# Performance work log

Measured on AMD Instinct MI355X. Metric: run time of the kernel, lower is better.

Reference implementation:

```python
import jax, jax.numpy as jnp
import numpy as np

N_ATOMS = 16384
APC = 64            # atoms per conformer
N_CONF = 256        # 64 mols * 4 confs
N_MOL = 64
DEG = 32
E = N_ATOMS * DEG
H = 128             # hidden_channels = num_filters = out_channels
G = 50              # num_gaussians
L = 6               # num_interactions
CUTOFF = 10.0
LOG2 = float(np.log(2.0))


def ssp(x):
    # ShiftedSoftplus: softplus(x) - log(2)
    return jax.nn.softplus(x) - LOG2


def setup_inputs() -> dict:
    key = jax.random.key(0)
    ks = jax.random.split(key, 24)
    rng = np.random.default_rng(0)

    z = jnp.asarray(rng.integers(1, 100, size=(N_ATOMS,)), dtype=jnp.int64 if jax.config.jax_enable_x64 else jnp.int32)
    # positions uniform in a 5A box -> all intra-conformer distances < cutoff
    pos = jax.random.uniform(ks[0], (N_ATOMS, 3), dtype=jnp.float32) * 5.0

    # within-conformer random edges, no self loops (radius_graph surrogate)
    i = np.repeat(np.arange(N_ATOMS), DEG)
    off = rng.integers(1, APC, size=E)
    j = (i // APC) * APC + (i % APC + off) % APC
    edge_index = jnp.asarray(np.stack([j, i]), dtype=jnp.int32)  # [2,E] (source, target)

    atom_to_conf = jnp.asarray(np.arange(N_ATOMS) // APC, dtype=jnp.int32)
    conf_to_mol = jnp.asarray(np.arange(N_CONF) // (N_CONF // N_MOL), dtype=jnp.int32)

    s = 0.05
    p = {
        'emb':     jax.random.normal(ks[1], (120, H), jnp.float32) * s,
        # per-interaction stacked params [L, ...]
        'mlp_w1':  jax.random.normal(ks[2], (L, G, H), jnp.float32) * s,
        'mlp_b1':  jnp.zeros((L, H), jnp.float32),
        'mlp_w2':  jax.random.normal(ks[3], (L, H, H), jnp.float32) * s,
        'mlp_b2':  jnp.zeros((L, H), jnp.float32),
        'cf_w1':   jax.random.normal(ks[4], (L, H, H), jnp.float32) * s,
        'cf_w2':   jax.random.normal(ks[5], (L, H, H), jnp.float32) * s,
        'cf_b2':   jnp.zeros((L, H), jnp.float32),
        'int_w':   jax.random.normal(ks[6], (L, H, H), jnp.float32) * s,
        'int_b':   jnp.zeros((L, H), jnp.float32),
        # readout head
        'out_w1':  jax.random.normal(ks[7], (H, H), jnp.float32) * s,
        'out_b1':  jnp.zeros((H,), jnp.float32),
        'out_w2':  jax.random.normal(ks[8], (H, H), jnp.float32) * s,
        'out_b2':  jnp.zeros((H,), jnp.float32),
        'head_w1': jax.random.normal(ks[9], (H, H // 2), jnp.float32) * s,
        'head_b1': jnp.zeros((H // 2,), jnp.float32),
        'head_w2': jax.random.normal(ks[10], (H // 2, 1), jnp.float32) * s,
        'head_b2': jnp.zeros((1,), jnp.float32),
    }
    return dict(z=z, pos=pos, edge_index=edge_index, atom_to_conf=atom_to_conf,
                conf_to_mol=conf_to_mol, **p)


def reference(z, pos, edge_index, atom_to_conf, conf_to_mol, emb,
              mlp_w1, mlp_b1, mlp_w2, mlp_b2, cf_w1, cf_w2, cf_b2,
              int_w, int_b, out_w1, out_b1, out_w2, out_b2,
              head_w1, head_b1, head_w2, head_b2):
    row, col = edge_index[0], edge_index[1]  # message from row, aggregated at col

    h = emb[z]                                             # [N,H]
    edge_weight = jnp.linalg.norm(pos[row] - pos[col], axis=-1)  # [E]

    # GaussianSmearing
    offset = jnp.linspace(0.0, CUTOFF, G)
    coeff = -0.5 / (offset[1] - offset[0]) ** 2
    edge_attr = jnp.exp(coeff * (edge_weight[:, None] - offset[None, :]) ** 2)  # [E,G]

    C = 0.5 * (jnp.cos(edge_weight * jnp.pi / CUTOFF) + 1.0)  # cosine cutoff [E]

    for l in range(L):
        # filter network on edge features, modulated by cutoff envelope
        Wf = ssp(edge_attr @ mlp_w1[l] + mlp_b1[l]) @ mlp_w2[l] + mlp_b2[l]
        Wf = Wf * C[:, None]                               # [E,H]
        xf = h @ cf_w1[l]                                  # lin1 (no bias) [N,H]
        msg = xf[row] * Wf                                 # gather * filter [E,H]
        agg = jax.ops.segment_sum(msg, col, num_segments=N_ATOMS)  # scatter-add [N,H]
        xc = agg @ cf_w2[l] + cf_b2[l]                     # lin2
        h = h + (ssp(xc) @ int_w[l] + int_b[l])            # act, lin, residual

    h = ssp(h @ out_w1 + out_b1)
    h = h @ out_w2 + out_b2                                # [N,H]

    conf_emb = jax.ops.segment_sum(h, atom_to_conf, num_segments=N_CONF)   # [C,H]
    mol_emb = jax.ops.segment_sum(conf_emb, conf_to_mol, num_segments=N_MOL)  # [M,H]

    out = (ssp(mol_emb @ head_w1 + head_b1) @ head_w2 + head_b2)[:, 0]  # [M]
    return out
```

## Files before the change

kernel.cpp:

```cpp
#include <hip/hip_runtime.h>
#include <math.h>

#define N_ATOMS 16384
#define APC 64
#define N_CONF 256
#define N_MOL 64
#define DEG 32
#define NEDGE (N_ATOMS * DEG)
#define H 128
#define G 50
#define NL 6
#define TP0 512
#define TPB 4096
#define CUTOFF 10.0f

typedef __attribute__((ext_vector_type(8))) short short8_t;
typedef __attribute__((ext_vector_type(4))) float f32x4;
typedef __attribute__((ext_vector_type(2))) float f32x2;

__device__ __forceinline__ float ssp_f(float x) {
  float e = __expf(-fabsf(x));
  return fmaxf(x, 0.f) + __logf(1.f + e) - 0.69314718055994531f;
}
__device__ __forceinline__ unsigned short bf16_rne(float x) {
  unsigned u = __float_as_uint(x);
  unsigned r = u + 0x7FFF + ((u >> 16) & 1);
  return (unsigned short)(r >> 16);
}
__device__ __forceinline__ float bf16_to_f(unsigned short s) {
  return __uint_as_float(((unsigned)s) << 16);
}
__device__ __forceinline__ float bflo(unsigned u) { return __uint_as_float(u << 16); }
__device__ __forceinline__ float bfhi(unsigned u) { return __uint_as_float(u & 0xFFFF0000u); }

__device__ __forceinline__ unsigned cvt_pk_bf16(float a, float b) {
  unsigned r;
  asm("v_cvt_pk_bf16_f32 %0, %1, %2" : "=v"(r) : "v"(a), "v"(b));
  return r;
}
__device__ __forceinline__ void pack4(const f32x4 v, uint2* hh, uint2* ll) {
  unsigned h01 = cvt_pk_bf16(v[0], v[1]);
  unsigned h23 = cvt_pk_bf16(v[2], v[3]);
  unsigned l01 = cvt_pk_bf16(v[0] - bflo(h01), v[1] - bfhi(h01));
  unsigned l23 = cvt_pk_bf16(v[2] - bflo(h23), v[3] - bfhi(h23));
  *hh = make_uint2(h01, h23);
  *ll = make_uint2(l01, l23);
}

__global__ __launch_bounds__(256) void k_setup(
    const float* __restrict__ pos, const int* __restrict__ esrc,
    const int* __restrict__ etgt, int* __restrict__ pk,
    const float* __restrict__ cf_w1, const float* __restrict__ cf_w2,
    const float* __restrict__ int_w, const float* __restrict__ out_w1,
    const float* __restrict__ out_w2, short* __restrict__ PW,
    const float* __restrict__ w1, const float* __restrict__ b1,
    const float* __restrict__ w2, const float* __restrict__ b2,
    float* __restrict__ T, int* __restrict__ cnt) {
  __shared__ float g2[2][64];
  __shared__ float S2[2][128];
  const int b = blockIdx.x;
  const int tid = threadIdx.x;
  if (b == 0 && tid == 0) *cnt = 0;
  if (b < 2048) {
    int e = b * 256 + tid;
    int r = esrc[e], c = etgt[e];
    float dx = pos[r * 3 + 0] - pos[c * 3 + 0];
    float dy = pos[r * 3 + 1] - pos[c * 3 + 1];
    float dz = pos[r * 3 + 2] - pos[c * 3 + 2];
    float d = sqrtf(dx * dx + dy * dy + dz * dz);
    int i = (int)(d * ((float)(TPB - 1) / CUTOFF) + 0.5f);
    if (i > TPB - 1) i = TPB - 1;
    if (i < 0) i = 0;
    pk[e] = (i << 8) | ((r & (APC - 1)) << 20);
  } else if (b < 2208) {
    int e = (b - 2048) * 256 + tid;
    int g = e >> 11, t = e & 2047;
    int kb = t >> 9, rem = t & 511, nt = rem >> 6, lane = rem & 63;
    int quad = lane >> 4, ln = lane & 15;
    int kbase = kb * 32 + quad * 8;
    int n = nt * 16 + ln;
    const float* src;
    if (g < 12) {
      int l = g >> 1;
      src = (g & 1) ? (int_w + l * 16384) : (cf_w2 + l * 16384);
    } else if (g < 18) {
      src = cf_w1 + (g - 12) * 16384;
    } else {
      src = (g == 18) ? out_w1 : out_w2;
    }
    short hv[8], lv[8];
    #pragma unroll
    for (int j = 0; j < 8; j++) {
      float x = src[(kbase + j) * H + n];
      unsigned short hb = bf16_rne(x);
      hv[j] = (short)hb;
      lv[j] = (short)bf16_rne(x - bf16_to_f(hb));
    }
    size_t base = (size_t)g * 32768 + (size_t)t * 8;
    *(short8_t*)&PW[base] = *(short8_t*)hv;
    *(short8_t*)&PW[base + 16384] = *(short8_t*)lv;
  } else {
    int bb = b - 2208;
    const int l = bb >> 8;
    const int grp = tid >> 7;
    const int c = tid & 127;
    const int p = (bb & 255) * 2 + grp;
    const float d = (float)p * (CUTOFF / (float)(TP0 - 1));
    const float gspace = CUTOFF / (float)(G - 1);
    const float coeff = -0.5f / (gspace * gspace);
    if (c < G) {
      float x = d - (float)c * gspace;
      g2[grp][c] = __expf(coeff * x * x);
    }
    __syncthreads();
    const float* W1 = w1 + l * G * H;
    float s = b1[l * H + c];
    #pragma unroll 5
    for (int i = 0; i < G; i++) s += g2[grp][i] * W1[i * H + c];
    S2[grp][c] = ssp_f(s);
    __syncthreads();
    const float* W2 = w2 + l * H * H;
    float o = b2[l * H + c];
    #pragma unroll 8
    for (int j = 0; j < H; j++) o += S2[grp][j] * W2[j * H + c];
    float Cc = 0.5f * (__cosf(d * (3.14159265358979f / CUTOFF)) + 1.f);
    T[((size_t)l * TP0 + p) * H + c] = o * Cc;
  }
}

__global__ __launch_bounds__(256) void k_up(const float* __restrict__ T,
                                            unsigned short* __restrict__ Tb) {
  int t = blockIdx.x * 256 + threadIdx.x;
  int l = t >> 17;
  int rem = t & 131071;
  int p4 = rem >> 5, cg = rem & 31;
  int c = cg * 4;
  float u = (float)p4 * ((float)(TP0 - 1) / (float)(TPB - 1));
  int i = (int)u;
  if (i > TP0 - 2) i = TP0 - 2;
  float f = u - (float)i;
  const float* a = T + ((size_t)l * TP0 + i) * H + c;
  float4 v0 = *(const float4*)a;
  float4 v1 = *(const float4*)(a + H);
  ushort4 o;
  o.x = bf16_rne(v0.x + f * (v1.x - v0.x));
  o.y = bf16_rne(v0.y + f * (v1.y - v0.y));
  o.z = bf16_rne(v0.z + f * (v1.z - v0.z));
  o.w = bf16_rne(v0.w + f * (v1.w - v0.w));
  int dst = (cg < 16) ? cg * 8 : (cg - 16) * 8 + 4;
  *(ushort4*)&Tb[((size_t)l * TPB + p4) * H + dst] = o;
}

#define MFMA(a, b, c) __builtin_amdgcn_mfma_f32_16x16x32_bf16((a), (b), (c), 0, 0, 0)

__device__ __forceinline__ void gemm_rt2(const short (*AH)[136], const short (*AL)[136],
                                         const short* __restrict__ pw,
                                         int rt2, int nt, int lane, int quad, int ln,
                                         f32x4 acc[2]) {
  #pragma unroll
  for (int kb = 0; kb < 4; kb++) {
    const short* pb = pw + ((size_t)(kb * 8 + nt) * 64 + lane) * 8;
    short8_t bh = *(const short8_t*)pb;
    short8_t bl = *(const short8_t*)(pb + 16384);
    int ko = kb * 32 + quad * 8;
    #pragma unroll
    for (int rtt = 0; rtt < 2; rtt++) {
      int row = rt2 * 32 + rtt * 16 + ln;
      short8_t ah = *(const short8_t*)&AH[row][ko];
      short8_t al = *(const short8_t*)&AL[row][ko];
      acc[rtt] = MFMA(ah, bh, acc[rtt]);
      acc[rtt] = MFMA(ah, bl, acc[rtt]);
      acc[rtt] = MFMA(al, bh, acc[rtt]);
    }
  }
}

__device__ __forceinline__ void gemm_rt2T(const short (*AH)[136], const short (*AL)[136],
                                          const short* __restrict__ pw,
                                          int rt2, int nt, int lane, int quad, int ln,
                                          f32x4 acc[2]) {
  #pragma unroll
  for (int kb = 0; kb < 4; kb++) {
    const short* pb = pw + ((size_t)(kb * 8 + nt) * 64 + lane) * 8;
    short8_t bh = *(const short8_t*)pb;
    short8_t bl = *(const short8_t*)(pb + 16384);
    int ko = kb * 32 + quad * 8;
    #pragma unroll
    for (int rtt = 0; rtt < 2; rtt++) {
      int row = rt2 * 32 + rtt * 16 + ln;
      short8_t ah = *(const short8_t*)&AH[row][ko];
      short8_t al = *(const short8_t*)&AL[row][ko];
      acc[rtt] = MFMA(bh, ah, acc[rtt]);
      acc[rtt] = MFMA(bl, ah, acc[rtt]);
      acc[rtt] = MFMA(bh, al, acc[rtt]);
    }
  }
}

__global__ __launch_bounds__(1024, 1) void k_mega(
    const int* __restrict__ z, const float* __restrict__ emb,
    const int* __restrict__ pk, const unsigned short* __restrict__ Tb,
    const short* __restrict__ PW, const float* __restrict__ cf_b2,
    const float* __restrict__ int_b, const float* __restrict__ out_b1,
    const float* __restrict__ out_b2, float* __restrict__ ce,
    const float* __restrict__ hw1, const float* __restrict__ hb1,
    const float* __restrict__ hw2, const float* __restrict__ hb2,
    int* __restrict__ cnt, float* __restrict__ outp) {
  __shared__ float xs[64][128];
  __shared__ __align__(16) short hH[64][136], hL[64][136];
  __shared__ __align__(16) short tH[64][136], tL[64][136];
  __shared__ __align__(16) short S1H[64][136], S1L[64][136];
  __shared__ int pks[2048];
  __shared__ float ps[2][128];
  __shared__ int is_last;
  const int conf = blockIdx.x;
  const int tid = threadIdx.x;
  const int lane = tid & 63, w = tid >> 6;
  const int quad = lane >> 4, ln = lane & 15;
  const int rt2 = w & 1, nt = w >> 1;
  const int eg = lane >> 4, c0 = (lane & 15) * 4;
  const int colb = nt * 16 + quad * 4;

  pks[tid] = pk[conf * 2048 + tid];
  pks[tid + 1024] = pk[conf * 2048 + 1024 + tid];

  {
    int r = tid >> 4, cb = (tid & 15) * 8;
    const float* src = emb + (size_t)z[conf * 64 + r] * H + cb;
    float4 v0 = *(const float4*)src, v1 = *(const float4*)(src + 4);
    float vv[8] = {v0.x, v0.y, v0.z, v0.w, v1.x, v1.y, v1.z, v1.w};
    short hv[8], lv[8];
    #pragma unroll
    for (int u = 0; u < 8; u++) {
      unsigned short hb = bf16_rne(vv[u]);
      hv[u] = (short)hb;
      lv[u] = (short)bf16_rne(vv[u] - bf16_to_f(hb));
    }
    *(short8_t*)&hH[r][cb] = *(short8_t*)hv;
    *(short8_t*)&hL[r][cb] = *(short8_t*)lv;
  }
  __syncthreads();

  {
    f32x4 acc[2] = {{0.f, 0.f, 0.f, 0.f}, {0.f, 0.f, 0.f, 0.f}};
    gemm_rt2T(hH, hL, PW + (size_t)12 * 32768, rt2, nt, lane, quad, ln, acc);
    #pragma unroll
    for (int rtt = 0; rtt < 2; rtt++)
      *(f32x4*)&xs[rt2 * 32 + rtt * 16 + ln][colb] = acc[rtt];
  }
  __syncthreads();

  for (int l = 0; l < NL; l++) {
    const char* Tlb = (const char*)(Tb + (size_t)l * TPB * H) + ln * 16;
    #pragma unroll 1
    for (int aa = 0; aa < 4; aa++) {
      int a2 = w * 4 + aa;
      int ms[8];
      uint4 tvv[8];
      #pragma unroll
      for (int it = 0; it < 8; it++) {
        ms[it] = pks[a2 * DEG + it * 4 + eg];
        tvv[it] = *(const uint4*)(Tlb + (ms[it] & 0xFFFFF));
      }
      f32x2 ac0 = {0.f, 0.f}, ac1 = {0.f, 0.f}, ac2 = {0.f, 0.f}, ac3 = {0.f, 0.f};
      #pragma unroll
      for (int it = 0; it < 8; it++) {
        int sl = ms[it] >> 20;
        const float* xr = &xs[sl][c0];
        float4 x0 = *(const float4*)xr;
        float4 x1 = *(const float4*)(xr + 64);
        uint4 tv = tvv[it];
        ac0 = __builtin_elementwise_fma((f32x2){bflo(tv.x), bfhi(tv.x)},
                                        (f32x2){x0.x, x0.y}, ac0);
        ac1 = __builtin_elementwise_fma((f32x2){bflo(tv.y), bfhi(tv.y)},
                                        (f32x2){x0.z, x0.w}, ac1);
        ac2 = __builtin_elementwise_fma((f32x2){bflo(tv.z), bfhi(tv.z)},
                                        (f32x2){x1.x, x1.y}, ac2);
        ac3 = __builtin_elementwise_fma((f32x2){bflo(tv.w), bfhi(tv.w)},
                                        (f32x2){x1.z, x1.w}, ac3);
      }
      float accs[8] = {ac0.x, ac0.y, ac1.x, ac1.y, ac2.x, ac2.y, ac3.x, ac3.y};
      #pragma unroll
      for (int j = 0; j < 8; j++) {
        accs[j] += __shfl_xor(accs[j], 16);
        accs[j] += __shfl_xor(accs[j], 32);
      }
      float va = eg == 0 ? accs[0] : eg == 1 ? accs[2] : eg == 2 ? accs[4] : accs[6];
      float vb = eg == 0 ? accs[1] : eg == 1 ? accs[3] : eg == 2 ? accs[5] : accs[7];
      unsigned short ha = bf16_rne(va), hb = bf16_rne(vb);
      unsigned short la = bf16_rne(va - bf16_to_f(ha));
      unsigned short lb = bf16_rne(vb - bf16_to_f(hb));
      int cw = (eg >> 1) * 64 + c0 + (eg & 1) * 2;
      *(short2*)&S1H[a2][cw] = make_short2((short)ha, (short)hb);
      *(short2*)&S1L[a2][cw] = make_short2((short)la, (short)lb);
    }
    __syncthreads();
    {
      f32x4 acc[2] = {{0.f, 0.f, 0.f, 0.f}, {0.f, 0.f, 0.f, 0.f}};
      gemm_rt2T(S1H, S1L, PW + (size_t)(2 * l) * 32768, rt2, nt, lane, quad, ln, acc);
      f32x4 bb4 = *(const f32x4*)&cf_b2[l * H + colb];
      #pragma unroll
      for (int rtt = 0; rtt < 2; rtt++) {
        int row = rt2 * 32 + rtt * 16 + ln;
        f32x4 v;
        #pragma unroll
        for (int reg = 0; reg < 4; reg++) v[reg] = ssp_f(acc[rtt][reg] + bb4[reg]);
        uint2 hh, ll;
        pack4(v, &hh, &ll);
        *(uint2*)&tH[row][colb] = hh;
        *(uint2*)&tL[row][colb] = ll;
      }
    }
    __syncthreads();
    {
      f32x4 acc[2] = {{0.f, 0.f, 0.f, 0.f}, {0.f, 0.f, 0.f, 0.f}};
      gemm_rt2T(tH, tL, PW + (size_t)(2 * l + 1) * 32768, rt2, nt, lane, quad, ln, acc);
      f32x4 bb4 = *(const f32x4*)&int_b[l * H + colb];
      #pragma unroll
      for (int rtt = 0; rtt < 2; rtt++) {
        int row = rt2 * 32 + rtt * 16 + ln;
        uint2 rh = *(const uint2*)&hH[row][colb];
        uint2 rl = *(const uint2*)&hL[row][colb];
        f32x4 v;
        v[0] = acc[rtt][0] + bb4[0] + bflo(rh.x) + bflo(rl.x);
        v[1] = acc[rtt][1] + bb4[1] + bfhi(rh.x) + bfhi(rl.x);
        v[2] = acc[rtt][2] + bb4[2] + bflo(rh.y) + bflo(rl.y);
        v[3] = acc[rtt][3] + bb4[3] + bfhi(rh.y) + bfhi(rl.y);
        uint2 hh, ll;
        pack4(v, &hh, &ll);
        *(uint2*)&hH[row][colb] = hh;
        *(uint2*)&hL[row][colb] = ll;
      }
    }
    __syncthreads();
    if (l < NL - 1) {
      f32x4 acc[2] = {{0.f, 0.f, 0.f, 0.f}, {0.f, 0.f, 0.f, 0.f}};
      gemm_rt2T(hH, hL, PW + (size_t)(13 + l) * 32768, rt2, nt, lane, quad, ln, acc);
      #pragma unroll
      for (int rtt = 0; rtt < 2; rtt++)
        *(f32x4*)&xs[rt2 * 32 + rtt * 16 + ln][colb] = acc[rtt];
      __syncthreads();
    }
  }

  {
    f32x4 acc[2] = {{0.f, 0.f, 0.f, 0.f}, {0.f, 0.f, 0.f, 0.f}};
    gemm_rt2T(hH, hL, PW + (size_t)18 * 32768, rt2, nt, lane, quad, ln, acc);
    f32x4 bb4 = *(const f32x4*)&out_b1[colb];
    #pragma unroll
    for (int rtt = 0; rtt < 2; rtt++) {
      int row = rt2 * 32 + rtt * 16 + ln;
      f32x4 v;
      #pragma unroll
      for (int reg = 0; reg < 4; reg++) v[reg] = ssp_f(acc[rtt][reg] + bb4[reg]);
      uint2 hh, ll;
      pack4(v, &hh, &ll);
      *(uint2*)&tH[row][colb] = hh;
      *(uint2*)&tL[row][colb] = ll;
    }
  }
  __syncthreads();
  {
    f32x4 acc[2] = {{0.f, 0.f, 0.f, 0.f}, {0.f, 0.f, 0.f, 0.f}};
    gemm_rt2(tH, tL, PW + (size_t)19 * 32768, rt2, nt, lane, quad, ln, acc);
    int col = nt * 16 + ln;
    float s = acc[0][0] + acc[0][1] + acc[0][2] + acc[0][3] +
              acc[1][0] + acc[1][1] + acc[1][2] + acc[1][3];
    s += __shfl_xor(s, 16);
    s += __shfl_xor(s, 32);
    if (quad == 0) ps[rt2][col] = s;
  }
  __syncthreads();
  if (tid < 128) {
    float v = ps[0][tid] + ps[1][tid] + 64.f * out_b2[tid];
    __hip_atomic_store(&ce[conf * 128 + tid], v, __ATOMIC_RELAXED,
                       __HIP_MEMORY_SCOPE_AGENT);
  }
  __syncthreads();
  if (tid == 0) {
    __threadfence();
    int old = __hip_atomic_fetch_add(cnt, 1, __ATOMIC_ACQ_REL,
                                     __HIP_MEMORY_SCOPE_AGENT);
    is_last = (old == N_CONF - 1) ? 1 : 0;
  }
  __syncthreads();
  if (is_last) {
    __threadfence();
    float* mol = &xs[0][0];
    for (int t = tid; t < N_MOL * 128; t += 1024) {
      int m = t >> 7, c = t & 127;
      const float* b = ce + (size_t)(m * 4) * 128;
      float s = __hip_atomic_load(&b[c], __ATOMIC_RELAXED, __HIP_MEMORY_SCOPE_AGENT) +
                __hip_atomic_load(&b[128 + c], __ATOMIC_RELAXED, __HIP_MEMORY_SCOPE_AGENT) +
                __hip_atomic_load(&b[256 + c], __ATOMIC_RELAXED, __HIP_MEMORY_SCOPE_AGENT) +
                __hip_atomic_load(&b[384 + c], __ATOMIC_RELAXED, __HIP_MEMORY_SCOPE_AGENT);
      mol[t] = s;
    }
    __syncthreads();
    float* q = (float*)&S1H[0][0];
    for (int t = tid; t < N_MOL * 64; t += 1024) {
      int m = t >> 6, j = t & 63;
      float qq = hb1[j];
      #pragma unroll 8
      for (int c = 0; c < H; c++) qq += mol[m * 128 + c] * hw1[c * 64 + j];
      q[t] = ssp_f(qq);
    }
    __syncthreads();
    if (tid < N_MOL) {
      float o = hb2[0];
      #pragma unroll 8
      for (int j = 0; j < 64; j++) o += q[tid * 64 + j] * hw2[j];
      outp[tid] = o;
    }
  }
}

extern "C" void kernel_launch(void* const* d_in, const int* in_sizes, int n_in,
                              void* d_out, int out_size, void* d_ws, size_t ws_size,
                              hipStream_t stream) {
  const int*   z       = (const int*)d_in[0];
  const float* pos     = (const float*)d_in[1];
  const int*   eidx    = (const int*)d_in[2];
  const float* emb     = (const float*)d_in[5];
  const float* mlp_w1  = (const float*)d_in[6];
  const float* mlp_b1  = (const float*)d_in[7];
  const float* mlp_w2  = (const float*)d_in[8];
  const float* mlp_b2  = (const float*)d_in[9];
  const float* cf_w1   = (const float*)d_in[10];
  const float* cf_w2   = (const float*)d_in[11];
  const float* cf_b2   = (const float*)d_in[12];
  const float* int_w   = (const float*)d_in[13];
  const float* int_b   = (const float*)d_in[14];
  const float* out_w1  = (const float*)d_in[15];
  const float* out_b1  = (const float*)d_in[16];
  const float* out_w2  = (const float*)d_in[17];
  const float* out_b2  = (const float*)d_in[18];
  const float* head_w1 = (const float*)d_in[19];
  const float* head_b1 = (const float*)d_in[20];
  const float* head_w2 = (const float*)d_in[21];
  const float* head_b2 = (const float*)d_in[22];

  char* ws = (char*)d_ws;
  float*          T   = (float*)ws;
  unsigned short* Tb  = (unsigned short*)(ws + (size_t)NL * TP0 * H * 4);
  char*           p2  = (char*)Tb + (size_t)NL * TPB * H * 2;
  int*            pk  = (int*)p2;
  short*          PW  = (short*)(p2 + (size_t)NEDGE * 4);
  float*          ce  = (float*)((char*)PW + (size_t)20 * 32768 * 2);
  int*            cnt = (int*)((char*)ce + (size_t)N_CONF * H * 4);

  k_setup<<<3744, 256, 0, stream>>>(pos, eidx, eidx + NEDGE, pk,
                                    cf_w1, cf_w2, int_w, out_w1, out_w2, PW,
                                    mlp_w1, mlp_b1, mlp_w2, mlp_b2, T, cnt);
  k_up<<<(NL * TPB * H / 4) / 256, 256, 0, stream>>>(T, Tb);

  k_mega<<<N_CONF, 1024, 0, stream>>>(z, emb, pk, Tb, PW, cf_b2, int_b,
                                      out_b1, out_b2, ce,
                                      head_w1, head_b1, head_w2, head_b2,
                                      cnt, (float*)d_out);
}
```

Baseline: 243.1 us.

## Prefetch GEMM weight fragments before barriers and first-atom filter gathers across layers

Weight fragments for each MFMA GEMM are now loaded into registers before the preceding __syncthreads, so global/L2 latency overlaps the barrier wait instead of sitting inside the GEMM. The first aggregation atom's packed-edge indices and filter-table rows for the next layer are also prefetched during the previous layer's xs GEMM. This hides gather latency at layer boundaries, at the cost of extra live registers (64 B-fragment shorts plus 8 uint4 per thread) under a 1024-thread launch bound.

```diff
diff --git a/kernel.cpp b/kernel.cpp
--- a/kernel.cpp
+++ b/kernel.cpp
@@ -153,49 +153,92 @@
 
 #define MFMA(a, b, c) __builtin_amdgcn_mfma_f32_16x16x32_bf16((a), (b), (c), 0, 0, 0)
 
+struct BF {
+  short8_t h[4];
+  short8_t l[4];
+};
+__device__ __forceinline__ BF load_B(const short* __restrict__ pw, int nt, int lane) {
+  BF b;
+  #pragma unroll
+  for (int kb = 0; kb < 4; kb++) {
+    const short* pb = pw + ((size_t)(kb * 8 + nt) * 64 + lane) * 8;
+    b.h[kb] = *(const short8_t*)pb;
+    b.l[kb] = *(const short8_t*)(pb + 16384);
+  }
+  return b;
+}
+
 __device__ __forceinline__ void gemm_rt2(const short (*AH)[136], const short (*AL)[136],
-                                         const short* __restrict__ pw,
-                                         int rt2, int nt, int lane, int quad, int ln,
+                                         const BF& b, int rt2, int quad, int ln,
                                          f32x4 acc[2]) {
   #pragma unroll
   for (int kb = 0; kb < 4; kb++) {
-    const short* pb = pw + ((size_t)(kb * 8 + nt) * 64 + lane) * 8;
-    short8_t bh = *(const short8_t*)pb;
-    short8_t bl = *(const short8_t*)(pb + 16384);
     int ko = kb * 32 + quad * 8;
     #pragma unroll
     for (int rtt = 0; rtt < 2; rtt++) {
       int row = rt2 * 32 + rtt * 16 + ln;
       short8_t ah = *(const short8_t*)&AH[row][ko];
       short8_t al = *(const short8_t*)&AL[row][ko];
-      acc[rtt] = MFMA(ah, bh, acc[rtt]);
-      acc[rtt] = MFMA(ah, bl, acc[rtt]);
-      acc[rtt] = MFMA(al, bh, acc[rtt]);
+      acc[rtt] = MFMA(ah, b.h[kb], acc[rtt]);
+      acc[rtt] = MFMA(ah, b.l[kb], acc[rtt]);
+      acc[rtt] = MFMA(al, b.h[kb], acc[rtt]);
     }
   }
 }
 
 __device__ __forceinline__ void gemm_rt2T(const short (*AH)[136], const short (*AL)[136],
-                                          const short* __restrict__ pw,
-                                          int rt2, int nt, int lane, int quad, int ln,
+                                          const BF& b, int rt2, int quad, int ln,
                                           f32x4 acc[2]) {
   #pragma unroll
   for (int kb = 0; kb < 4; kb++) {
-    const short* pb = pw + ((size_t)(kb * 8 + nt) * 64 + lane) * 8;
-    short8_t bh = *(const short8_t*)pb;
-    short8_t bl = *(const short8_t*)(pb + 16384);
     int ko = kb * 32 + quad * 8;
     #pragma unroll
     for (int rtt = 0; rtt < 2; rtt++) {
       int row = rt2 * 32 + rtt * 16 + ln;
       short8_t ah = *(const short8_t*)&AH[row][ko];
       short8_t al = *(const short8_t*)&AL[row][ko];
-      acc[rtt] = MFMA(bh, ah, acc[rtt]);
-      acc[rtt] = MFMA(bl, ah, acc[rtt]);
-      acc[rtt] = MFMA(bh, al, acc[rtt]);
-    }
-  }
-}
+      acc[rtt] = MFMA(b.h[kb], ah, acc[rtt]);
+      acc[rtt] = MFMA(b.l[kb], ah, acc[rtt]);
+      acc[rtt] = MFMA(b.h[kb], al, acc[rtt]);
+    }
+  }
+}
+
+#define AGG_BODY(A2, MSARR, TVARR)                                             \
+  {                                                                            \
+    f32x2 ac0 = {0.f, 0.f}, ac1 = {0.f, 0.f}, ac2 = {0.f, 0.f},                \
+          ac3 = {0.f, 0.f};                                                    \
+    _Pragma("unroll") for (int it = 0; it < 8; it++) {                         \
+      int sl = MSARR[it] >> 20;                                                \
+      const float* xr = &xs[sl][c0];                                           \
+      float4 x0 = *(const float4*)xr;                                          \
+      float4 x1 = *(const float4*)(xr + 64);                                   \
+      uint4 tv = TVARR[it];                                                    \
+      ac0 = __builtin_elementwise_fma((f32x2){bflo(tv.x), bfhi(tv.x)},         \
+                                      (f32x2){x0.x, x0.y}, ac0);               \
+      ac1 = __builtin_elementwise_fma((f32x2){bflo(tv.y), bfhi(tv.y)},         \
+                                      (f32x2){x0.z, x0.w}, ac1);               \
+      ac2 = __builtin_elementwise_fma((f32x2){bflo(tv.z), bfhi(tv.z)},         \
+                                      (f32x2){x1.x, x1.y}, ac2);               \
+      ac3 = __builtin_elementwise_fma((f32x2){bflo(tv.w), bfhi(tv.w)},         \
+                                      (f32x2){x1.z, x1.w}, ac3);               \
+    }                                                                          \
+    float accs[8] = {ac0.x, ac0.y, ac1.x, ac1.y, ac2.x, ac2.y, ac3.x, ac3.y};  \
+    _Pragma("unroll") for (int j = 0; j < 8; j++) {                            \
+      accs[j] += __shfl_xor(accs[j], 16);                                      \
+      accs[j] += __shfl_xor(accs[j], 32);                                      \
+    }                                                                          \
+    float va =                                                                 \
+        eg == 0 ? accs[0] : eg == 1 ? accs[2] : eg == 2 ? accs[4] : accs[6];   \
+    float vb =                                                                 \
+        eg == 0 ? accs[1] : eg == 1 ? accs[3] : eg == 2 ? accs[5] : accs[7];   \
+    unsigned short ha = bf16_rne(va), hb = bf16_rne(vb);                       \
+    unsigned short la = bf16_rne(va - bf16_to_f(ha));                          \
+    unsigned short lb = bf16_rne(vb - bf16_to_f(hb));                          \
+    int cw = (eg >> 1) * 64 + c0 + (eg & 1) * 2;                               \
+    *(short2*)&S1H[A2][cw] = make_short2((short)ha, (short)hb);                \
+    *(short2*)&S1L[A2][cw] = make_short2((short)la, (short)lb);                \
+  }
 
 __global__ __launch_bounds__(1024, 1) void k_mega(
     const int* __restrict__ z, const float* __restrict__ emb,
@@ -239,21 +282,36 @@
     *(short8_t*)&hH[r][cb] = *(short8_t*)hv;
     *(short8_t*)&hL[r][cb] = *(short8_t*)lv;
   }
-  __syncthreads();
+  BF bX = load_B(PW + (size_t)12 * 32768, nt, lane);
+  __syncthreads();
+
+  int msP[8];
+  uint4 tvP[8];
 
   {
     f32x4 acc[2] = {{0.f, 0.f, 0.f, 0.f}, {0.f, 0.f, 0.f, 0.f}};
-    gemm_rt2T(hH, hL, PW + (size_t)12 * 32768, rt2, nt, lane, quad, ln, acc);
+    gemm_rt2T(hH, hL, bX, rt2, quad, ln, acc);
     #pragma unroll
     for (int rtt = 0; rtt < 2; rtt++)
       *(f32x4*)&xs[rt2 * 32 + rtt * 16 + ln][colb] = acc[rtt];
   }
-  __syncthreads();
+  {
+    const char* T0 = (const char*)Tb + ln * 16;
+    #pragma unroll
+    for (int it = 0; it < 8; it++) {
+      msP[it] = pks[(w * 4) * DEG + it * 4 + eg];
+      tvP[it] = *(const uint4*)(T0 + (msP[it] & 0xFFFFF));
+    }
+  }
+  __syncthreads();
+
+  BF bN;
 
   for (int l = 0; l < NL; l++) {
     const char* Tlb = (const char*)(Tb + (size_t)l * TPB * H) + ln * 16;
+    AGG_BODY(w * 4, msP, tvP)
     #pragma unroll 1
-    for (int aa = 0; aa < 4; aa++) {
+    for (int aa = 1; aa < 4; aa++) {
       int a2 = w * 4 + aa;
       int ms[8];
       uint4 tvv[8];
@@ -262,42 +320,13 @@
         ms[it] = pks[a2 * DEG + it * 4 + eg];
         tvv[it] = *(const uint4*)(Tlb + (ms[it] & 0xFFFFF));
       }
-      f32x2 ac0 = {0.f, 0.f}, ac1 = {0.f, 0.f}, ac2 = {0.f, 0.f}, ac3 = {0.f, 0.f};
-      #pragma unroll
-      for (int it = 0; it < 8; it++) {
-        int sl = ms[it] >> 20;
-        const float* xr = &xs[sl][c0];
-        float4 x0 = *(const float4*)xr;
-        float4 x1 = *(const float4*)(xr + 64);
-        uint4 tv = tvv[it];
-        ac0 = __builtin_elementwise_fma((f32x2){bflo(tv.x), bfhi(tv.x)},
-                                        (f32x2){x0.x, x0.y}, ac0);
-        ac1 = __builtin_elementwise_fma((f32x2){bflo(tv.y), bfhi(tv.y)},
-                                        (f32x2){x0.z, x0.w}, ac1);
-        ac2 = __builtin_elementwise_fma((f32x2){bflo(tv.z), bfhi(tv.z)},
-                                        (f32x2){x1.x, x1.y}, ac2);
-        ac3 = __builtin_elementwise_fma((f32x2){bflo(tv.w), bfhi(tv.w)},
-                                        (f32x2){x1.z, x1.w}, ac3);
-      }
-      float accs[8] = {ac0.x, ac0.y, ac1.x, ac1.y, ac2.x, ac2.y, ac3.x, ac3.y};
-      #pragma unroll
-      for (int j = 0; j < 8; j++) {
-        accs[j] += __shfl_xor(accs[j], 16);
-        accs[j] += __shfl_xor(accs[j], 32);
-      }
-      float va = eg == 0 ? accs[0] : eg == 1 ? accs[2] : eg == 2 ? accs[4] : accs[6];
-      float vb = eg == 0 ? accs[1] : eg == 1 ? accs[3] : eg == 2 ? accs[5] : accs[7];
-      unsigned short ha = bf16_rne(va), hb = bf16_rne(vb);
-      unsigned short la = bf16_rne(va - bf16_to_f(ha));
-      unsigned short lb = bf16_rne(vb - bf16_to_f(hb));
-      int cw = (eg >> 1) * 64 + c0 + (eg & 1) * 2;
-      *(short2*)&S1H[a2][cw] = make_short2((short)ha, (short)hb);
-      *(short2*)&S1L[a2][cw] = make_short2((short)la, (short)lb);
-    }
+      AGG_BODY(a2, ms, tvv)
+    }
+    bN = load_B(PW + (size_t)(2 * l) * 32768, nt, lane);
     __syncthreads();
     {
       f32x4 acc[2] = {{0.f, 0.f, 0.f, 0.f}, {0.f, 0.f, 0.f, 0.f}};
-      gemm_rt2T(S1H, S1L, PW + (size_t)(2 * l) * 32768, rt2, nt, lane, quad, ln, acc);
+      gemm_rt2T(S1H, S1L, bN, rt2, quad, ln, acc);
       f32x4 bb4 = *(const f32x4*)&cf_b2[l * H + colb];
       #pragma unroll
       for (int rtt = 0; rtt < 2; rtt++) {
@@ -311,10 +340,11 @@
         *(uint2*)&tL[row][colb] = ll;
       }
     }
+    bN = load_B(PW + (size_t)(2 * l + 1) * 32768, nt, lane);
     __syncthreads();
     {
       f32x4 acc[2] = {{0.f, 0.f, 0.f, 0.f}, {0.f, 0.f, 0.f, 0.f}};
-      gemm_rt2T(tH, tL, PW + (size_t)(2 * l + 1) * 32768, rt2, nt, lane, quad, ln, acc);
+      gemm_rt2T(tH, tL, bN, rt2, quad, ln, acc);
       f32x4 bb4 = *(const f32x4*)&int_b[l * H + colb];
       #pragma unroll
       for (int rtt = 0; rtt < 2; rtt++) {
@@ -332,20 +362,27 @@
         *(uint2*)&hL[row][colb] = ll;
       }
     }
+    bN = load_B(PW + (size_t)((l < NL - 1) ? (13 + l) : 18) * 32768, nt, lane);
     __syncthreads();
     if (l < NL - 1) {
       f32x4 acc[2] = {{0.f, 0.f, 0.f, 0.f}, {0.f, 0.f, 0.f, 0.f}};
-      gemm_rt2T(hH, hL, PW + (size_t)(13 + l) * 32768, rt2, nt, lane, quad, ln, acc);
+      gemm_rt2T(hH, hL, bN, rt2, quad, ln, acc);
       #pragma unroll
       for (int rtt = 0; rtt < 2; rtt++)
         *(f32x4*)&xs[rt2 * 32 + rtt * 16 + ln][colb] = acc[rtt];
+      const char* Tn = (const char*)(Tb + (size_t)(l + 1) * TPB * H) + ln * 16;
+      #pragma unroll
+      for (int it = 0; it < 8; it++) {
+        msP[it] = pks[(w * 4) * DEG + it * 4 + eg];
+        tvP[it] = *(const uint4*)(Tn + (msP[it] & 0xFFFFF));
+      }
       __syncthreads();
     }
   }
 
   {
     f32x4 acc[2] = {{0.f, 0.f, 0.f, 0.f}, {0.f, 0.f, 0.f, 0.f}};
-    gemm_rt2T(hH, hL, PW + (size_t)18 * 32768, rt2, nt, lane, quad, ln, acc);
+    gemm_rt2T(hH, hL, bN, rt2, quad, ln, acc);
     f32x4 bb4 = *(const f32x4*)&out_b1[colb];
     #pragma unroll
     for (int rtt = 0; rtt < 2; rtt++) {
@@ -359,10 +396,11 @@
       *(uint2*)&tL[row][colb] = ll;
     }
   }
+  bN = load_B(PW + (size_t)19 * 32768, nt, lane);
   __syncthreads();
   {
     f32x4 acc[2] = {{0.f, 0.f, 0.f, 0.f}, {0.f, 0.f, 0.f, 0.f}};
-    gemm_rt2(tH, tL, PW + (size_t)19 * 32768, rt2, nt, lane, quad, ln, acc);
+    gemm_rt2(tH, tL, bN, rt2, quad, ln, acc);
     int col = nt * 16 + ln;
     float s = acc[0][0] + acc[0][1] + acc[0][2] + acc[0][3] +
               acc[1][0] + acc[1][1] + acc[1][2] + acc[1][3];
```

Result: faster. 234.5 us (-3.5%).
